# Performance work log

Hardware: AMD Instinct MI355X
Metric: run time of the kernel (lower is better)

The kernel has to match this reference:

```python
import jax, jax.numpy as jnp
import numpy as np

B, N, E, IDX = 4, 200000, 128, 2048


def setup_inputs() -> dict:
    key = jax.random.key(0)
    ks = jax.random.split(key, 6)
    x = jax.random.normal(ks[0], (B, N, E), dtype=jnp.float32)
    mask = jax.random.randint(ks[1], (B, N), 0, 2).astype(jnp.int32)
    index = jax.random.randint(ks[2], (B, N), 0, IDX).astype(jnp.int32)
    W = jax.random.normal(ks[3], (E, E), dtype=jnp.float32) * 0.05
    b = jax.random.normal(ks[4], (E,), dtype=jnp.float32) * 0.05
    context = jax.random.normal(ks[5], (E,), dtype=jnp.float32)
    return {"x": x, "W": W, "b": b, "context": context, "mask": mask, "index": index}


def _segment_attend(scores, idx, xb):
    # scores: [N], idx: [N] int, xb: [N, E]
    m = jax.ops.segment_max(scores, idx, num_segments=IDX)  # [IDX]
    m = jnp.where(jnp.isfinite(m), m, 0.0)  # empty segments -> -inf guard
    e = jnp.exp(scores - m[idx])
    ssum = jax.ops.segment_sum(e, idx, num_segments=IDX)  # [IDX]
    w = e / ssum[idx]  # segment softmax weights, [N]
    out = jax.ops.segment_sum(xb * w[:, None], idx, num_segments=IDX)  # [IDX, E]
    return out, w


def reference(x, W, b, context, mask, index):
    norm = jnp.sqrt(jnp.asarray(E, dtype=x.dtype))
    hidden = jnp.tanh(jnp.einsum('bne,fe->bnf', x, W) + b)  # Linear(E,E) + tanh
    importance = jnp.einsum('bne,e->bn', hidden, context) / norm
    importance = jnp.where(mask == 0, jnp.asarray(-1e9, dtype=x.dtype), importance)
    out, attn = jax.vmap(_segment_attend)(importance, index, x)
    return out, attn
```

## Files before the change

kernel.cpp:

```cpp
#include <hip/hip_runtime.h>
#include <hip/hip_bf16.h>
#include <math.h>

#define B_    4
#define N_    200000
#define E_    128
#define IDX_  2048
#define TT    (B_*N_)
#define INV_NORM 0.08838834764831845f
#define CAP   512
#define WPAD  136

typedef __attribute__((ext_vector_type(8))) short bf16x8;
typedef __attribute__((ext_vector_type(4))) float f32x4;

__device__ __forceinline__ unsigned short f2bf(float f) {
    unsigned int u = __float_as_uint(f);
    unsigned int r = (u + 0x7fffu + ((u >> 16) & 1u)) >> 16;
    return (unsigned short)r;
}

__global__ __launch_bounds__(256) void score_kernel(
    const float* __restrict__ x, const float* __restrict__ W,
    const float* __restrict__ bias, const float* __restrict__ ctx,
    const int* __restrict__ mask, const int* __restrict__ index,
    float* __restrict__ scores, int* __restrict__ counts)
{
    __shared__ unsigned short Wb[E_ * WPAD];

    const int tid = threadIdx.x;

    for (int i = tid; i < E_ * E_ / 4; i += 256) {
        int f = i >> 5, kb = (i & 31) * 4;
        float4 v = ((const float4*)W)[i];
        ushort4 o;
        o.x = f2bf(v.x); o.y = f2bf(v.y); o.z = f2bf(v.z); o.w = f2bf(v.w);
        *(ushort4*)&Wb[f * WPAD + kb] = o;
    }
    __syncthreads();

    const int lane = tid & 63;
    const int col  = lane & 15;
    const int q    = lane >> 4;
    const int wave = tid >> 6;

    float ctx_r[8], bias2[8], csum = 0.f;
#pragma unroll
    for (int n = 0; n < 8; n++) {
        ctx_r[n] = ctx[n * 16 + col];
        bias2[n] = 2.f * bias[n * 16 + col];
        csum += ctx_r[n];
    }
    const float csum_n = csum * INV_NORM;

    bf16x8 Bf[8][4];
#pragma unroll
    for (int n = 0; n < 8; n++)
#pragma unroll
        for (int kt = 0; kt < 4; kt++)
            Bf[n][kt] = *(const bf16x8*)&Wb[(n * 16 + col) * WPAD + kt * 32 + q * 8];

    for (long base0 = (long)blockIdx.x * 64; base0 < TT; base0 += (long)gridDim.x * 64) {
        const long tbase = base0 + wave * 16;
        const float* xrow = x + (tbase + col) * (long)E_;

        bf16x8 Af[4];
#pragma unroll
        for (int kt = 0; kt < 4; kt++) {
            float4 u = ((const float4*)xrow)[kt * 8 + q * 2];
            float4 v = ((const float4*)xrow)[kt * 8 + q * 2 + 1];
            union { bf16x8 vec; __hip_bfloat162 h[4]; } a;
            a.h[0] = __float22bfloat162_rn(make_float2(u.x, u.y));
            a.h[1] = __float22bfloat162_rn(make_float2(u.z, u.w));
            a.h[2] = __float22bfloat162_rn(make_float2(v.x, v.y));
            a.h[3] = __float22bfloat162_rn(make_float2(v.z, v.w));
            Af[kt] = a.vec;
        }

        f32x4 acc[8];
#pragma unroll
        for (int n = 0; n < 8; n++) acc[n] = (f32x4){0.f, 0.f, 0.f, 0.f};

#pragma unroll
        for (int kt = 0; kt < 4; kt++)
#pragma unroll
            for (int n = 0; n < 8; n++)
                acc[n] = __builtin_amdgcn_mfma_f32_16x16x32_bf16(Af[kt], Bf[n][kt], acc[n], 0, 0, 0);

        float pr[4];
#pragma unroll
        for (int r = 0; r < 4; r++) {
            float psum = 0.f;
#pragma unroll
            for (int n = 0; n < 8; n++) {
                float t = fmaf(acc[n][r], 2.f, bias2[n]);
                float rc = __builtin_amdgcn_rcpf(1.f + __expf(t));
                psum = fmaf(ctx_r[n], rc, psum);
            }
            float p = fmaf(-2.f * INV_NORM, psum, csum_n);
#pragma unroll
            for (int o = 1; o < 16; o <<= 1) p += __shfl_xor(p, o);
            pr[r] = p;
        }
        if (col == 0) {
            int4 mv = ((const int4*)(mask + tbase))[q];
            float4 s;
            s.x = mv.x ? pr[0] : -1e9f;
            s.y = mv.y ? pr[1] : -1e9f;
            s.z = mv.z ? pr[2] : -1e9f;
            s.w = mv.w ? pr[3] : -1e9f;
            ((float4*)(scores + tbase))[q] = s;

            int4 iv = ((const int4*)(index + tbase))[q];
            int* cb = counts + (int)(tbase / N_) * IDX_;
            atomicAdd(&cb[iv.x], 1);
            atomicAdd(&cb[iv.y], 1);
            atomicAdd(&cb[iv.z], 1);
            atomicAdd(&cb[iv.w], 1);
        }
    }
}

__global__ __launch_bounds__(1024) void scan_kernel(
    const int* __restrict__ counts, int* __restrict__ offsets, int* __restrict__ cursor)
{
    __shared__ int sums[1024];
    int tid = threadIdx.x;
    int c[8], loc[8], s = 0;
#pragma unroll
    for (int j = 0; j < 8; j++) { c[j] = counts[tid * 8 + j]; loc[j] = s; s += c[j]; }
    sums[tid] = s;
    __syncthreads();
    for (int off = 1; off < 1024; off <<= 1) {
        int v = (tid >= off) ? sums[tid - off] : 0;
        __syncthreads();
        if (tid >= off) sums[tid] += v;
        __syncthreads();
    }
    int base = (tid > 0) ? sums[tid - 1] : 0;
#pragma unroll
    for (int j = 0; j < 8; j++) {
        int o = base + loc[j];
        offsets[tid * 8 + j] = o;
        cursor[tid * 8 + j]  = o;
    }
}

__global__ void scatter_kernel(const int* __restrict__ index, int* __restrict__ cursor,
                               int* __restrict__ tokenlist)
{
    for (int tok = blockIdx.x * blockDim.x + threadIdx.x; tok < TT;
         tok += gridDim.x * blockDim.x) {
        int b = tok / N_;
        int pos = atomicAdd(&cursor[b * IDX_ + index[tok]], 1);
        tokenlist[pos] = tok;
    }
}

__global__ __launch_bounds__(256) void attend_kernel(
    const float* __restrict__ x, const int* __restrict__ counts,
    const int* __restrict__ offsets, const int* __restrict__ tokenlist,
    float* __restrict__ attn , float* __restrict__ out)
{
    const int key   = blockIdx.x;
    const int tid   = threadIdx.x;
    const int e     = tid & 127;
    const int slice = tid >> 7;
    const int cnt   = counts[key];
    const int off   = offsets[key];

    if (cnt == 0) { if (slice == 0) out[(size_t)key * E_ + e] = 0.f; return; }

    __shared__ int   toks[CAP];
    __shared__ float wv[CAP];
    __shared__ float rbuf[4];
    __shared__ float part[E_];

    if (cnt <= CAP) {
        float m = -INFINITY;
        for (int j = tid; j < cnt; j += 256) {
            int t = tokenlist[off + j];
            float s = attn[t];
            toks[j] = t; wv[j] = s;
            m = fmaxf(m, s);
        }
#pragma unroll
        for (int o = 32; o > 0; o >>= 1) m = fmaxf(m, __shfl_xor(m, o));
        if ((tid & 63) == 0) rbuf[tid >> 6] = m;
        __syncthreads();
        m = fmaxf(fmaxf(rbuf[0], rbuf[1]), fmaxf(rbuf[2], rbuf[3]));
        __syncthreads();

        float sum = 0.f;
        for (int j = tid; j < cnt; j += 256) {
            float ev = __expf(wv[j] - m);
            wv[j] = ev;
            sum += ev;
        }
#pragma unroll
        for (int o = 32; o > 0; o >>= 1) sum += __shfl_xor(sum, o);
        if ((tid & 63) == 0) rbuf[tid >> 6] = sum;
        __syncthreads();
        float inv = 1.f / (rbuf[0] + rbuf[1] + rbuf[2] + rbuf[3]);

        for (int j = tid; j < cnt; j += 256) {
            float w = wv[j] * inv;
            wv[j] = w;
            attn[toks[j]] = w;
        }
        __syncthreads();

        float acc = 0.f;
        int j = slice;
        for (; j + 6 < cnt; j += 8) {
            int   t0 = toks[j],   t1 = toks[j+2], t2 = toks[j+4], t3 = toks[j+6];
            float w0 = wv[j],     w1 = wv[j+2],   w2 = wv[j+4],   w3 = wv[j+6];
            float x0 = x[(size_t)t0 * E_ + e];
            float x1 = x[(size_t)t1 * E_ + e];
            float x2 = x[(size_t)t2 * E_ + e];
            float x3 = x[(size_t)t3 * E_ + e];
            acc = fmaf(w0, x0, acc);
            acc = fmaf(w1, x1, acc);
            acc = fmaf(w2, x2, acc);
            acc = fmaf(w3, x3, acc);
        }
        for (; j < cnt; j += 2) acc = fmaf(wv[j], x[(size_t)toks[j] * E_ + e], acc);

        if (slice == 1) part[e] = acc;
        __syncthreads();
        if (slice == 0) out[(size_t)key * E_ + e] = acc + part[e];
    } else {
        float m = -INFINITY;
        for (int j = tid; j < cnt; j += 256) m = fmaxf(m, attn[tokenlist[off + j]]);
#pragma unroll
        for (int o = 32; o > 0; o >>= 1) m = fmaxf(m, __shfl_xor(m, o));
        if ((tid & 63) == 0) rbuf[tid >> 6] = m;
        __syncthreads();
        m = fmaxf(fmaxf(rbuf[0], rbuf[1]), fmaxf(rbuf[2], rbuf[3]));
        __syncthreads();

        float sum = 0.f;
        for (int j = tid; j < cnt; j += 256) sum += __expf(attn[tokenlist[off + j]] - m);
#pragma unroll
        for (int o = 32; o > 0; o >>= 1) sum += __shfl_xor(sum, o);
        if ((tid & 63) == 0) rbuf[tid >> 6] = sum;
        __syncthreads();
        float inv = 1.f / (rbuf[0] + rbuf[1] + rbuf[2] + rbuf[3]);
        __syncthreads();

        for (int j = tid; j < cnt; j += 256) {
            int t = tokenlist[off + j];
            attn[t] = __expf(attn[t] - m) * inv;
        }
        __threadfence();
        __syncthreads();

        float acc = 0.f;
        for (int j = slice; j < cnt; j += 2) {
            int t = tokenlist[off + j];
            acc = fmaf(attn[t], x[(size_t)t * E_ + e], acc);
        }
        if (slice == 1) part[e] = acc;
        __syncthreads();
        if (slice == 0) out[(size_t)key * E_ + e] = acc + part[e];
    }
}

extern "C" void kernel_launch(void* const* d_in, const int* in_sizes, int n_in,
                              void* d_out, int out_size, void* d_ws, size_t ws_size,
                              hipStream_t stream)
{
    const float* x    = (const float*)d_in[0];
    const float* W    = (const float*)d_in[1];
    const float* bias = (const float*)d_in[2];
    const float* ctx  = (const float*)d_in[3];
    const int*   mask = (const int*)d_in[4];
    const int*   index= (const int*)d_in[5];

    float* out  = (float*)d_out;
    float* attn = out + (size_t)B_ * IDX_ * E_;

    int* counts    = (int*)d_ws;
    int* offsets   = counts  + B_ * IDX_;
    int* cursor    = offsets + B_ * IDX_;
    int* tokenlist = cursor  + B_ * IDX_;

    hipMemsetAsync(counts, 0, B_ * IDX_ * sizeof(int), stream);
    score_kernel  <<<2048, 256, 0, stream>>>(x, W, bias, ctx, mask, index, attn, counts);
    scan_kernel   <<<1, 1024, 0, stream>>>(counts, offsets, cursor);
    scatter_kernel<<<1024, 256, 0, stream>>>(index, cursor, tokenlist);
    attend_kernel <<<B_ * IDX_, 256, 0, stream>>>(x, counts, offsets, tokenlist, attn, out);
}
```

Baseline: 736.4 us.

## Pack score with token id and assign one wave per segment in attend

The scatter pass now stores (token, score) pairs, so the attend kernel reads scores contiguously instead of gathering attn[t] at random. The attend kernel maps one 64-lane wave to each segment (four segments per block), keeps softmax values in registers and uses wave shuffles instead of block barriers. Each lane reads float2 so a single wave covers a full 128-float row. This doubles the token list footprint and gives each segment less parallelism, so segments that are large or uneven in size take longer per wave.

```diff
diff --git a/kernel.cpp b/kernel.cpp
--- a/kernel.cpp
+++ b/kernel.cpp
@@ -9,6 +9,7 @@
 #define TT    (B_*N_)
 #define INV_NORM 0.08838834764831845f
 #define CAP   512
+#define RCAP  8
 #define WPAD  136
 
 typedef __attribute__((ext_vector_type(8))) short bf16x8;
@@ -146,123 +147,132 @@
     }
 }
 
-__global__ void scatter_kernel(const int* __restrict__ index, int* __restrict__ cursor,
-                               int* __restrict__ tokenlist)
+__global__ __launch_bounds__(256) void scatter_kernel(
+    const int* __restrict__ index, const float* __restrict__ scores,
+    int* __restrict__ cursor, int2* __restrict__ tokenlist)
 {
     for (int tok = blockIdx.x * blockDim.x + threadIdx.x; tok < TT;
          tok += gridDim.x * blockDim.x) {
-        int b = tok / N_;
-        int pos = atomicAdd(&cursor[b * IDX_ + index[tok]], 1);
-        tokenlist[pos] = tok;
+        int seg = index[tok];
+        float s = scores[tok];
+        int b   = tok / N_;
+        int pos = atomicAdd(&cursor[b * IDX_ + seg], 1);
+        tokenlist[pos] = make_int2(tok, __float_as_int(s));
     }
 }
 
 __global__ __launch_bounds__(256) void attend_kernel(
     const float* __restrict__ x, const int* __restrict__ counts,
-    const int* __restrict__ offsets, const int* __restrict__ tokenlist,
+    const int* __restrict__ offsets, const int2* __restrict__ tokenlist,
     float* __restrict__ attn , float* __restrict__ out)
 {
-    const int key   = blockIdx.x;
-    const int tid   = threadIdx.x;
-    const int e     = tid & 127;
-    const int slice = tid >> 7;
-    const int cnt   = counts[key];
-    const int off   = offsets[key];
-
-    if (cnt == 0) { if (slice == 0) out[(size_t)key * E_ + e] = 0.f; return; }
-
-    __shared__ int   toks[CAP];
-    __shared__ float wv[CAP];
-    __shared__ float rbuf[4];
-    __shared__ float part[E_];
+    const int wave = threadIdx.x >> 6;
+    const int lane = threadIdx.x & 63;
+    const int key  = blockIdx.x * 4 + wave;
+    const int cnt  = counts[key];
+    const int off  = offsets[key];
+    const float2* __restrict__ x2 = (const float2*)x;
+    float2* out2 = (float2*)(out + (size_t)key * E_);
+
+    __shared__ int2 pair[4][CAP];
+
+    if (cnt == 0) { out2[lane] = make_float2(0.f, 0.f); return; }
 
     if (cnt <= CAP) {
+        int   tk[RCAP];
+        float sc[RCAP], ev[RCAP];
         float m = -INFINITY;
-        for (int j = tid; j < cnt; j += 256) {
-            int t = tokenlist[off + j];
-            float s = attn[t];
-            toks[j] = t; wv[j] = s;
-            m = fmaxf(m, s);
-        }
-#pragma unroll
-        for (int o = 32; o > 0; o >>= 1) m = fmaxf(m, __shfl_xor(m, o));
-        if ((tid & 63) == 0) rbuf[tid >> 6] = m;
-        __syncthreads();
-        m = fmaxf(fmaxf(rbuf[0], rbuf[1]), fmaxf(rbuf[2], rbuf[3]));
-        __syncthreads();
+#pragma unroll
+        for (int u = 0; u < RCAP; u++) {
+            int j = lane + u * 64;
+            if (j < cnt) {
+                int2 p = tokenlist[off + j];
+                tk[u] = p.x;
+                sc[u] = __int_as_float(p.y);
+                m = fmaxf(m, sc[u]);
+            }
+        }
+#pragma unroll
+        for (int o = 32; o; o >>= 1) m = fmaxf(m, __shfl_xor(m, o));
 
         float sum = 0.f;
-        for (int j = tid; j < cnt; j += 256) {
-            float ev = __expf(wv[j] - m);
-            wv[j] = ev;
-            sum += ev;
-        }
-#pragma unroll
-        for (int o = 32; o > 0; o >>= 1) sum += __shfl_xor(sum, o);
-        if ((tid & 63) == 0) rbuf[tid >> 6] = sum;
-        __syncthreads();
-        float inv = 1.f / (rbuf[0] + rbuf[1] + rbuf[2] + rbuf[3]);
-
-        for (int j = tid; j < cnt; j += 256) {
-            float w = wv[j] * inv;
-            wv[j] = w;
-            attn[toks[j]] = w;
-        }
-        __syncthreads();
-
-        float acc = 0.f;
-        int j = slice;
-        for (; j + 6 < cnt; j += 8) {
-            int   t0 = toks[j],   t1 = toks[j+2], t2 = toks[j+4], t3 = toks[j+6];
-            float w0 = wv[j],     w1 = wv[j+2],   w2 = wv[j+4],   w3 = wv[j+6];
-            float x0 = x[(size_t)t0 * E_ + e];
-            float x1 = x[(size_t)t1 * E_ + e];
-            float x2 = x[(size_t)t2 * E_ + e];
-            float x3 = x[(size_t)t3 * E_ + e];
-            acc = fmaf(w0, x0, acc);
-            acc = fmaf(w1, x1, acc);
-            acc = fmaf(w2, x2, acc);
-            acc = fmaf(w3, x3, acc);
-        }
-        for (; j < cnt; j += 2) acc = fmaf(wv[j], x[(size_t)toks[j] * E_ + e], acc);
-
-        if (slice == 1) part[e] = acc;
-        __syncthreads();
-        if (slice == 0) out[(size_t)key * E_ + e] = acc + part[e];
+#pragma unroll
+        for (int u = 0; u < RCAP; u++) {
+            int j = lane + u * 64;
+            if (j < cnt) { ev[u] = __expf(sc[u] - m); sum += ev[u]; }
+        }
+#pragma unroll
+        for (int o = 32; o; o >>= 1) sum += __shfl_xor(sum, o);
+        const float inv = 1.f / sum;
+
+#pragma unroll
+        for (int u = 0; u < RCAP; u++) {
+            int j = lane + u * 64;
+            if (j < cnt) {
+                float w = ev[u] * inv;
+                attn[tk[u]] = w;
+                pair[wave][j] = make_int2(tk[u], __float_as_int(w));
+            }
+        }
+
+        float2 acc = make_float2(0.f, 0.f);
+        int j = 0;
+        for (; j + 3 < cnt; j += 4) {
+            int2 p0 = pair[wave][j];
+            int2 p1 = pair[wave][j + 1];
+            int2 p2 = pair[wave][j + 2];
+            int2 p3 = pair[wave][j + 3];
+            float2 a0 = x2[(size_t)p0.x * 64 + lane];
+            float2 a1 = x2[(size_t)p1.x * 64 + lane];
+            float2 a2 = x2[(size_t)p2.x * 64 + lane];
+            float2 a3 = x2[(size_t)p3.x * 64 + lane];
+            float w0 = __int_as_float(p0.y), w1 = __int_as_float(p1.y);
+            float w2 = __int_as_float(p2.y), w3 = __int_as_float(p3.y);
+            acc.x = fmaf(w0, a0.x, acc.x); acc.y = fmaf(w0, a0.y, acc.y);
+            acc.x = fmaf(w1, a1.x, acc.x); acc.y = fmaf(w1, a1.y, acc.y);
+            acc.x = fmaf(w2, a2.x, acc.x); acc.y = fmaf(w2, a2.y, acc.y);
+            acc.x = fmaf(w3, a3.x, acc.x); acc.y = fmaf(w3, a3.y, acc.y);
+        }
+        for (; j < cnt; j++) {
+            int2  p = pair[wave][j];
+            float2 a = x2[(size_t)p.x * 64 + lane];
+            float w = __int_as_float(p.y);
+            acc.x = fmaf(w, a.x, acc.x); acc.y = fmaf(w, a.y, acc.y);
+        }
+        out2[lane] = acc;
     } else {
         float m = -INFINITY;
-        for (int j = tid; j < cnt; j += 256) m = fmaxf(m, attn[tokenlist[off + j]]);
-#pragma unroll
-        for (int o = 32; o > 0; o >>= 1) m = fmaxf(m, __shfl_xor(m, o));
-        if ((tid & 63) == 0) rbuf[tid >> 6] = m;
-        __syncthreads();
-        m = fmaxf(fmaxf(rbuf[0], rbuf[1]), fmaxf(rbuf[2], rbuf[3]));
-        __syncthreads();
+        for (int j = lane; j < cnt; j += 64)
+            m = fmaxf(m, __int_as_float(tokenlist[off + j].y));
+#pragma unroll
+        for (int o = 32; o; o >>= 1) m = fmaxf(m, __shfl_xor(m, o));
 
         float sum = 0.f;
-        for (int j = tid; j < cnt; j += 256) sum += __expf(attn[tokenlist[off + j]] - m);
-#pragma unroll
-        for (int o = 32; o > 0; o >>= 1) sum += __shfl_xor(sum, o);
-        if ((tid & 63) == 0) rbuf[tid >> 6] = sum;
-        __syncthreads();
-        float inv = 1.f / (rbuf[0] + rbuf[1] + rbuf[2] + rbuf[3]);
-        __syncthreads();
-
-        for (int j = tid; j < cnt; j += 256) {
-            int t = tokenlist[off + j];
-            attn[t] = __expf(attn[t] - m) * inv;
-        }
-        __threadfence();
-        __syncthreads();
-
-        float acc = 0.f;
-        for (int j = slice; j < cnt; j += 2) {
-            int t = tokenlist[off + j];
-            acc = fmaf(attn[t], x[(size_t)t * E_ + e], acc);
-        }
-        if (slice == 1) part[e] = acc;
-        __syncthreads();
-        if (slice == 0) out[(size_t)key * E_ + e] = acc + part[e];
+        for (int j = lane; j < cnt; j += 64)
+            sum += __expf(__int_as_float(tokenlist[off + j].y) - m);
+#pragma unroll
+        for (int o = 32; o; o >>= 1) sum += __shfl_xor(sum, o);
+        const float inv = 1.f / sum;
+
+        float2 acc = make_float2(0.f, 0.f);
+        for (int j0 = 0; j0 < cnt; j0 += 64) {
+            int t = 0; float w = 0.f;
+            if (j0 + lane < cnt) {
+                int2 p = tokenlist[off + j0 + lane];
+                t = p.x;
+                w = __expf(__int_as_float(p.y) - m) * inv;
+                attn[t] = w;
+            }
+            int lim = min(64, cnt - j0);
+            for (int jj = 0; jj < lim; jj++) {
+                int   tb = __shfl(t, jj);
+                float wb = __shfl(w, jj);
+                float2 a = x2[(size_t)tb * 64 + lane];
+                acc.x = fmaf(wb, a.x, acc.x);
+                acc.y = fmaf(wb, a.y, acc.y);
+            }
+        }
+        out2[lane] = acc;
     }
 }
 
@@ -283,11 +293,11 @@
     int* counts    = (int*)d_ws;
     int* offsets   = counts  + B_ * IDX_;
     int* cursor    = offsets + B_ * IDX_;
-    int* tokenlist = cursor  + B_ * IDX_;
+    int2* tokenlist = (int2*)(cursor + B_ * IDX_);
 
     hipMemsetAsync(counts, 0, B_ * IDX_ * sizeof(int), stream);
     score_kernel  <<<2048, 256, 0, stream>>>(x, W, bias, ctx, mask, index, attn, counts);
     scan_kernel   <<<1, 1024, 0, stream>>>(counts, offsets, cursor);
-    scatter_kernel<<<1024, 256, 0, stream>>>(index, cursor, tokenlist);
-    attend_kernel <<<B_ * IDX_, 256, 0, stream>>>(x, counts, offsets, tokenlist, attn, out);
-}
+    scatter_kernel<<<1024, 256, 0, stream>>>(index, attn, cursor, tokenlist);
+    attend_kernel <<<B_ * IDX_ / 4, 256, 0, stream>>>(x, counts, offsets, tokenlist, attn, out);
+}
```

Result: no change. 735.3 us (-0.1%).
